# Optimization experiments

Hardware: AMD Instinct MI355X
Metric: run time of the kernel (lower is better)

Reference implementation:

```python
import jax, jax.numpy as jnp
import numpy as np

N, D, K, H, G = 200000, 256, 128, 4, 1024  # nodes, emb_dim, hidden, heads, graphs


def setup_inputs() -> dict:
    key = jax.random.key(0)
    k0, k1, k2, k3 = jax.random.split(key, 4)
    node_features = jax.random.normal(k0, (N, D), jnp.float32)
    segment_ids = jnp.sort(jax.random.randint(k1, (N,), 0, G)).astype(jnp.int32)
    W1 = jax.random.normal(k2, (H, D, K), jnp.float32) / np.float32(np.sqrt(D))
    b1 = jnp.zeros((H, K), jnp.float32)
    W2 = jax.random.normal(k3, (H, K), jnp.float32) / np.float32(np.sqrt(K))
    b2 = jnp.zeros((H,), jnp.float32)
    return {"node_features": node_features, "segment_ids": segment_ids,
            "num_graphs": G, "W1": W1, "b1": b1, "W2": W2, "b2": b2}


def _segment_softmax(scores, seg, num_segments):
    # scores: [N, H]; numerically-stable softmax within each graph segment, per head
    m = jax.ops.segment_max(scores, seg, num_segments=num_segments)  # [G, H]
    e = jnp.exp(scores - m[seg])
    s = jax.ops.segment_sum(e, seg, num_segments=num_segments)  # [G, H]
    return e / s[seg]


def reference(node_features, segment_ids, num_graphs, W1, b1, W2, b2):
    # Per-head MLP score for all heads at once: [N, H]
    h = jax.nn.relu(jnp.einsum('nd,hdk->nhk', node_features, W1) + b1)
    scores = jnp.einsum('nhk,hk->nh', h, W2) + b2
    # dgl.softmax_nodes per head == segment softmax over graph ids
    attn = _segment_softmax(scores, segment_ids, num_graphs)  # [N, H]
    # combine_type == 'mean': mean_h segment_sum(attn_h * x)
    # == segment_sum(mean_h(attn_h) * x) since the sum is linear in attn.
    avg_attn = attn.mean(axis=1)  # [N]
    weighted = avg_attn[:, None] * node_features  # [N, D]
    return jax.ops.segment_sum(weighted, segment_ids, num_segments=num_graphs)  # [G, D]
```

## Files before the change

### kernel.cpp

```cpp
#include <hip/hip_runtime.h>
#include <hip/hip_bf16.h>

typedef unsigned short u16;
typedef __attribute__((ext_vector_type(8))) __bf16 bf16x8;
typedef __attribute__((ext_vector_type(8))) u16 u16x8;
typedef __attribute__((ext_vector_type(4))) float f32x4;

__device__ __forceinline__ u16 f2bf(float f) {
    unsigned u = __float_as_uint(f);
    u += 0x7fffu + ((u >> 16) & 1u);
    return (u16)(u >> 16);
}

__device__ __forceinline__ void gl_lds16(const void* g, void* l) {
    __builtin_amdgcn_global_load_lds(
        (const __attribute__((address_space(1))) void*)g,
        (__attribute__((address_space(3))) void*)l, 16, 0, 0);
}

__device__ __forceinline__ bf16x8 cvt8(f32x4 lo, f32x4 hi) {
    u16x8 u;
    u[0] = f2bf(lo[0]); u[1] = f2bf(lo[1]); u[2] = f2bf(lo[2]); u[3] = f2bf(lo[3]);
    u[4] = f2bf(hi[0]); u[5] = f2bf(hi[1]); u[6] = f2bf(hi[2]); u[7] = f2bf(hi[3]);
    return __builtin_bit_cast(bf16x8, u);
}

__global__ __launch_bounds__(256) void transpose_w1(const float* __restrict__ W1,
                                                    u16* __restrict__ W1T) {
    int idx = blockIdx.x * 256 + threadIdx.x;
    int h = idx >> 15;
    int rem = idx & 32767;
    int k = rem >> 8;
    int d = rem & 255;
    float v = W1[((size_t)h * 256 + d) * 128 + k];
    W1T[idx] = f2bf(v);
}

__global__ __launch_bounds__(256, 3) void score_kernel(
        const float* __restrict__ x, const u16* __restrict__ W1T,
        const float* __restrict__ b1, const float* __restrict__ W2,
        const float* __restrict__ b2, float* __restrict__ scores, int N) {
    __shared__ char sA[2][8192];
    __shared__ char sB[2][16384];
    __shared__ float red[2][128];

    const int t = threadIdx.x;
    const int wave = t >> 6;
    const int lane = t & 63;
    const int l15 = lane & 15;
    const int quad = lane >> 4;
    const int n0 = blockIdx.x * 128;
    const int h = blockIdx.y;
    const int valid = min(128, N - n0);

    const char* Abase = (const char*)(W1T + (size_t)h * 128 * 256);
    const char* Xbase = (const char*)x;

    f32x4 acc[4][4] = {};
    const int wr = (wave & 1) * 64;
    const int wn = (wave >> 1) * 64;

    auto stage = [&](int it, int buf) {
        const int k0 = it * 32;
#pragma unroll
        for (int j = 0; j < 2; ++j) {
            int s = j * 256 + t;
            int r = s >> 2, c = s & 3;
            const char* g = Abase + (size_t)r * 512 + k0 * 2 + ((c ^ ((r >> 1) & 3)) * 16);
            gl_lds16(g, &sA[buf][j * 4096 + wave * 1024]);
        }
#pragma unroll
        for (int j = 0; j < 4; ++j) {
            int s = j * 256 + t;
            int n = s >> 3, c = s & 7;
            int nn = n0 + n; if (nn >= N) nn = N - 1;
            const char* g = Xbase + (size_t)nn * 1024 + k0 * 4 + ((c ^ (n & 7)) * 16);
            gl_lds16(g, &sB[buf][j * 4096 + wave * 1024]);
        }
    };

    stage(0, 0);
    __syncthreads();

    for (int it = 0; it < 8; ++it) {
        if (it < 7) stage(it + 1, (it + 1) & 1);
        const int buf = it & 1;
        bf16x8 a[4], b[4];
#pragma unroll
        for (int rt = 0; rt < 4; ++rt) {
            int rl = wr + rt * 16 + l15;
            a[rt] = *reinterpret_cast<const bf16x8*>(
                &sA[buf][rl * 64 + ((quad ^ ((rl >> 1) & 3)) * 16)]);
        }
#pragma unroll
        for (int nt = 0; nt < 4; ++nt) {
            int nl = wn + nt * 16 + l15;
            f32x4 lo = *reinterpret_cast<const f32x4*>(
                &sB[buf][nl * 128 + (((2 * quad) ^ (nl & 7)) * 16)]);
            f32x4 hi = *reinterpret_cast<const f32x4*>(
                &sB[buf][nl * 128 + (((2 * quad + 1) ^ (nl & 7)) * 16)]);
            b[nt] = cvt8(lo, hi);
        }
#pragma unroll
        for (int rt = 0; rt < 4; ++rt)
#pragma unroll
            for (int nt = 0; nt < 4; ++nt)
                acc[rt][nt] = __builtin_amdgcn_mfma_f32_16x16x32_bf16(
                    a[rt], b[nt], acc[rt][nt], 0, 0, 0);
        __syncthreads();
    }

    float part[4] = {0.f, 0.f, 0.f, 0.f};
#pragma unroll
    for (int rt = 0; rt < 4; ++rt) {
        int rb = wr + rt * 16 + quad * 4;
        float4 w2v = *reinterpret_cast<const float4*>(W2 + h * 128 + rb);
        float4 b1v = *reinterpret_cast<const float4*>(b1 + h * 128 + rb);
#pragma unroll
        for (int nt = 0; nt < 4; ++nt) {
            f32x4 c = acc[rt][nt];
            part[nt] += fmaxf(c[0] + b1v.x, 0.f) * w2v.x
                      + fmaxf(c[1] + b1v.y, 0.f) * w2v.y
                      + fmaxf(c[2] + b1v.z, 0.f) * w2v.z
                      + fmaxf(c[3] + b1v.w, 0.f) * w2v.w;
        }
    }
#pragma unroll
    for (int nt = 0; nt < 4; ++nt) {
        float p = part[nt];
        p += __shfl_xor(p, 16, 64);
        p += __shfl_xor(p, 32, 64);
        if (lane < 16) red[wave & 1][wn + nt * 16 + l15] = p;
    }
    __syncthreads();
    if (t < valid)
        scores[(size_t)(n0 + t) * 4 + h] = red[0][t] + red[1][t] + b2[h];
}

__device__ __forceinline__ int lower_bound(const int* __restrict__ a, int n, int v) {
    int lo = 0, hi = n;
    while (lo < hi) {
        int mid = (lo + hi) >> 1;
        if (a[mid] < v) lo = mid + 1; else hi = mid;
    }
    return lo;
}

__global__ __launch_bounds__(256) void segstat_kernel(
        const float4* __restrict__ scores4, const int* __restrict__ seg,
        float4* __restrict__ mOut, float4* __restrict__ isOut, int N) {
    __shared__ float4 redm[4];
    __shared__ float4 reds[4];
    const int g = blockIdx.x;
    const int t = threadIdx.x;
    const int start = lower_bound(seg, N, g);
    const int end = lower_bound(seg, N, g + 1);

    float4 mx = make_float4(-3.4e38f, -3.4e38f, -3.4e38f, -3.4e38f);
    for (int i = start + t; i < end; i += 256) {
        float4 s = scores4[i];
        mx.x = fmaxf(mx.x, s.x); mx.y = fmaxf(mx.y, s.y);
        mx.z = fmaxf(mx.z, s.z); mx.w = fmaxf(mx.w, s.w);
    }
#pragma unroll
    for (int off = 1; off < 64; off <<= 1) {
        mx.x = fmaxf(mx.x, __shfl_xor(mx.x, off, 64));
        mx.y = fmaxf(mx.y, __shfl_xor(mx.y, off, 64));
        mx.z = fmaxf(mx.z, __shfl_xor(mx.z, off, 64));
        mx.w = fmaxf(mx.w, __shfl_xor(mx.w, off, 64));
    }
    if ((t & 63) == 0) redm[t >> 6] = mx;
    __syncthreads();
    mx = redm[0];
#pragma unroll
    for (int w = 1; w < 4; ++w) {
        mx.x = fmaxf(mx.x, redm[w].x); mx.y = fmaxf(mx.y, redm[w].y);
        mx.z = fmaxf(mx.z, redm[w].z); mx.w = fmaxf(mx.w, redm[w].w);
    }

    float4 sm = make_float4(0.f, 0.f, 0.f, 0.f);
    for (int i = start + t; i < end; i += 256) {
        float4 s = scores4[i];
        sm.x += expf(s.x - mx.x); sm.y += expf(s.y - mx.y);
        sm.z += expf(s.z - mx.z); sm.w += expf(s.w - mx.w);
    }
#pragma unroll
    for (int off = 1; off < 64; off <<= 1) {
        sm.x += __shfl_xor(sm.x, off, 64);
        sm.y += __shfl_xor(sm.y, off, 64);
        sm.z += __shfl_xor(sm.z, off, 64);
        sm.w += __shfl_xor(sm.w, off, 64);
    }
    if ((t & 63) == 0) reds[t >> 6] = sm;
    __syncthreads();
    if (t == 0) {
        float4 tot = reds[0];
        for (int w = 1; w < 4; ++w) {
            tot.x += reds[w].x; tot.y += reds[w].y;
            tot.z += reds[w].z; tot.w += reds[w].w;
        }
        bool nonempty = end > start;
        float4 m_out = nonempty ? mx : make_float4(0.f, 0.f, 0.f, 0.f);
        float4 is;
        is.x = (nonempty && tot.x > 0.f) ? 1.f / tot.x : 0.f;
        is.y = (nonempty && tot.y > 0.f) ? 1.f / tot.y : 0.f;
        is.z = (nonempty && tot.z > 0.f) ? 1.f / tot.z : 0.f;
        is.w = (nonempty && tot.w > 0.f) ? 1.f / tot.w : 0.f;
        mOut[g] = m_out;
        isOut[g] = is;
    }
}

__global__ __launch_bounds__(256) void wsum_kernel(
        const float* __restrict__ x, const float4* __restrict__ scores4,
        const int* __restrict__ seg, const float4* __restrict__ mArr,
        const float4* __restrict__ isArr, float* __restrict__ out, int N) {
    __shared__ float wl[256];
    __shared__ int gl[256];
    __shared__ unsigned long long bmask[4];
    const int t = threadIdx.x;
    const int n0 = blockIdx.x * 256;
    const int cnt = min(256, N - n0);

    int g = -1;
    float w = 0.f;
    if (t < cnt) {
        int n = n0 + t;
        g = seg[n];
        float4 s = scores4[n];
        float4 m = mArr[g];
        float4 is = isArr[g];
        w = 0.25f * (expf(s.x - m.x) * is.x + expf(s.y - m.y) * is.y +
                     expf(s.z - m.z) * is.z + expf(s.w - m.w) * is.w);
    }
    gl[t] = g;
    wl[t] = w;
    __syncthreads();
    bool bnd = (t > 0) && (t < cnt) && (gl[t] != gl[t - 1]);
    unsigned long long bm = __ballot(bnd);
    if ((t & 63) == 0) bmask[t >> 6] = bm;
    __syncthreads();

    int rs = 0;
    while (rs < cnt) {
        int re = cnt;
        {
            int wd = (rs + 1) >> 6, bb = (rs + 1) & 63;
            for (; wd < 4; ++wd, bb = 0) {
                unsigned long long mm = bmask[wd];
                if (bb) mm &= (~0ULL) << bb;
                if (mm) { re = wd * 64 + (__ffsll(mm) - 1); break; }
            }
            if (re > cnt) re = cnt;
        }
        float acc = 0.f;
        int i = rs;
        for (; i + 8 <= re; i += 8) {
            float xv[8];
#pragma unroll
            for (int j = 0; j < 8; ++j)
                xv[j] = x[(size_t)(n0 + i + j) * 256 + t];
#pragma unroll
            for (int j = 0; j < 8; ++j) acc += wl[i + j] * xv[j];
        }
        for (; i < re; ++i) acc += wl[i] * x[(size_t)(n0 + i) * 256 + t];
        atomicAdd(&out[(size_t)gl[rs] * 256 + t], acc);
        rs = re;
    }
}

extern "C" void kernel_launch(void* const* d_in, const int* in_sizes, int n_in,
                              void* d_out, int out_size, void* d_ws, size_t ws_size,
                              hipStream_t stream) {
    const float* x  = (const float*)d_in[0];
    const int* seg  = (const int*)d_in[1];
    const float* W1 = (const float*)d_in[3];
    const float* b1 = (const float*)d_in[4];
    const float* W2 = (const float*)d_in[5];
    const float* b2 = (const float*)d_in[6];
    float* out = (float*)d_out;

    const int N = in_sizes[0] / 256;
    const int G = 1024;

    char* ws = (char*)d_ws;
    float* scores = (float*)ws;
    u16* W1T      = (u16*)(ws + (size_t)N * 16);
    float* mArr   = (float*)(ws + (size_t)N * 16 + 262144);
    float* isArr  = mArr + (size_t)G * 4;

    hipMemsetAsync(d_out, 0, (size_t)G * 256 * sizeof(float), stream);
    transpose_w1<<<512, 256, 0, stream>>>(W1, W1T);
    dim3 sgrid((N + 127) / 128, 4);
    score_kernel<<<sgrid, 256, 0, stream>>>(x, W1T, b1, W2, b2, scores, N);
    segstat_kernel<<<G, 256, 0, stream>>>((const float4*)scores, seg,
                                          (float4*)mArr, (float4*)isArr, N);
    wsum_kernel<<<(N + 255) / 256, 256, 0, stream>>>(x, (const float4*)scores, seg,
                                                     (const float4*)mArr,
                                                     (const float4*)isArr, out, N);
}
```

Baseline: 423.2 us.

## Restructure score GEMM to load x once for all heads, retile wsum

The score kernel now handles 64 nodes per block across all four heads at once, one wave per head. Each block converts its x tile to bf16 a single time in LDS and streams all of W1T through LDS. The old kernel launched one block per head and so read and converted x four times. The W1 transpose now goes through an LDS tile for coalesced access, and wsum uses 64-node blocks with a single ballot mask, which gives more blocks and more atomics.

```diff
diff --git a/kernel.cpp b/kernel.cpp
--- a/kernel.cpp
+++ b/kernel.cpp
@@ -18,123 +18,135 @@
         (__attribute__((address_space(3))) void*)l, 16, 0, 0);
 }
 
-__device__ __forceinline__ bf16x8 cvt8(f32x4 lo, f32x4 hi) {
-    u16x8 u;
-    u[0] = f2bf(lo[0]); u[1] = f2bf(lo[1]); u[2] = f2bf(lo[2]); u[3] = f2bf(lo[3]);
-    u[4] = f2bf(hi[0]); u[5] = f2bf(hi[1]); u[6] = f2bf(hi[2]); u[7] = f2bf(hi[3]);
-    return __builtin_bit_cast(bf16x8, u);
-}
-
 __global__ __launch_bounds__(256) void transpose_w1(const float* __restrict__ W1,
                                                     u16* __restrict__ W1T) {
-    int idx = blockIdx.x * 256 + threadIdx.x;
-    int h = idx >> 15;
-    int rem = idx & 32767;
-    int k = rem >> 8;
-    int d = rem & 255;
-    float v = W1[((size_t)h * 256 + d) * 128 + k];
-    W1T[idx] = f2bf(v);
-}
-
-__global__ __launch_bounds__(256, 3) void score_kernel(
+    __shared__ u16 tile[64][132];
+    const int t = threadIdx.x;
+    const int h = blockIdx.x >> 2;
+    const int dt = blockIdx.x & 3;
+#pragma unroll
+    for (int j = 0; j < 8; ++j) {
+        int idx = j * 256 + t;
+        int r = idx >> 5;
+        int kq = idx & 31;
+        float4 v = *reinterpret_cast<const float4*>(
+            W1 + ((size_t)h * 256 + dt * 64 + r) * 128 + kq * 4);
+        ushort4 o;
+        o.x = f2bf(v.x); o.y = f2bf(v.y); o.z = f2bf(v.z); o.w = f2bf(v.w);
+        *reinterpret_cast<ushort4*>(&tile[r][kq * 4]) = o;
+    }
+    __syncthreads();
+#pragma unroll
+    for (int j = 0; j < 4; ++j) {
+        int idx = j * 256 + t;
+        int k = idx >> 3;
+        int c8 = idx & 7;
+        u16x8 o;
+#pragma unroll
+        for (int e = 0; e < 8; ++e) o[e] = tile[c8 * 8 + e][k];
+        *reinterpret_cast<u16x8*>(W1T + ((size_t)h * 128 + k) * 256 + dt * 64 + c8 * 8) = o;
+    }
+}
+
+__global__ __launch_bounds__(256, 2) void score_kernel(
         const float* __restrict__ x, const u16* __restrict__ W1T,
         const float* __restrict__ b1, const float* __restrict__ W2,
         const float* __restrict__ b2, float* __restrict__ scores, int N) {
-    __shared__ char sA[2][8192];
-    __shared__ char sB[2][16384];
-    __shared__ float red[2][128];
+    __shared__ u16 xb[16384];
+    __shared__ u16 sA[16384];
 
     const int t = threadIdx.x;
     const int wave = t >> 6;
     const int lane = t & 63;
     const int l15 = lane & 15;
     const int quad = lane >> 4;
-    const int n0 = blockIdx.x * 128;
-    const int h = blockIdx.y;
-    const int valid = min(128, N - n0);
-
-    const char* Abase = (const char*)(W1T + (size_t)h * 128 * 256);
-    const char* Xbase = (const char*)x;
-
-    f32x4 acc[4][4] = {};
-    const int wr = (wave & 1) * 64;
-    const int wn = (wave >> 1) * 64;
-
-    auto stage = [&](int it, int buf) {
-        const int k0 = it * 32;
-#pragma unroll
-        for (int j = 0; j < 2; ++j) {
-            int s = j * 256 + t;
-            int r = s >> 2, c = s & 3;
-            const char* g = Abase + (size_t)r * 512 + k0 * 2 + ((c ^ ((r >> 1) & 3)) * 16);
-            gl_lds16(g, &sA[buf][j * 4096 + wave * 1024]);
-        }
-#pragma unroll
-        for (int j = 0; j < 4; ++j) {
-            int s = j * 256 + t;
-            int n = s >> 3, c = s & 7;
-            int nn = n0 + n; if (nn >= N) nn = N - 1;
-            const char* g = Xbase + (size_t)nn * 1024 + k0 * 4 + ((c ^ (n & 7)) * 16);
-            gl_lds16(g, &sB[buf][j * 4096 + wave * 1024]);
+    const int n0 = blockIdx.x * 64;
+
+    {
+        const int nrow = wave * 16 + (lane >> 2);
+        const int koff = (lane & 3) * 8;
+        int nn = n0 + nrow; if (nn >= N) nn = N - 1;
+        const float* src = x + (size_t)nn * 256 + koff;
+        float4 v[16];
+#pragma unroll
+        for (int i = 0; i < 8; ++i) {
+            v[2 * i]     = *reinterpret_cast<const float4*>(src + i * 32);
+            v[2 * i + 1] = *reinterpret_cast<const float4*>(src + i * 32 + 4);
+        }
+#pragma unroll
+        for (int i = 0; i < 8; ++i) {
+            u16x8 o;
+            o[0] = f2bf(v[2*i].x);   o[1] = f2bf(v[2*i].y);
+            o[2] = f2bf(v[2*i].z);   o[3] = f2bf(v[2*i].w);
+            o[4] = f2bf(v[2*i+1].x); o[5] = f2bf(v[2*i+1].y);
+            o[6] = f2bf(v[2*i+1].z); o[7] = f2bf(v[2*i+1].w);
+            *reinterpret_cast<u16x8*>(&xb[(i * 256 + t) * 8]) = o;
+        }
+    }
+
+    const int arr = (lane >> 2);
+    const int akc = (lane & 3) * 8;
+    auto stageA = [&](int ks) {
+        const int k0 = ks * 32;
+#pragma unroll
+        for (int j = 0; j < 8; ++j) {
+            int fr = wave * 8 + j;
+            const u16* g = W1T + (size_t)(fr * 16 + arr) * 256 + k0 + akc;
+            gl_lds16(g, &sA[(size_t)fr * 512]);
         }
     };
 
-    stage(0, 0);
-    __syncthreads();
-
-    for (int it = 0; it < 8; ++it) {
-        if (it < 7) stage(it + 1, (it + 1) & 1);
-        const int buf = it & 1;
-        bf16x8 a[4], b[4];
-#pragma unroll
-        for (int rt = 0; rt < 4; ++rt) {
-            int rl = wr + rt * 16 + l15;
-            a[rt] = *reinterpret_cast<const bf16x8*>(
-                &sA[buf][rl * 64 + ((quad ^ ((rl >> 1) & 3)) * 16)]);
-        }
-#pragma unroll
-        for (int nt = 0; nt < 4; ++nt) {
-            int nl = wn + nt * 16 + l15;
-            f32x4 lo = *reinterpret_cast<const f32x4*>(
-                &sB[buf][nl * 128 + (((2 * quad) ^ (nl & 7)) * 16)]);
-            f32x4 hi = *reinterpret_cast<const f32x4*>(
-                &sB[buf][nl * 128 + (((2 * quad + 1) ^ (nl & 7)) * 16)]);
-            b[nt] = cvt8(lo, hi);
-        }
-#pragma unroll
-        for (int rt = 0; rt < 4; ++rt)
-#pragma unroll
-            for (int nt = 0; nt < 4; ++nt)
-                acc[rt][nt] = __builtin_amdgcn_mfma_f32_16x16x32_bf16(
-                    a[rt], b[nt], acc[rt][nt], 0, 0, 0);
+    f32x4 acc[8][4] = {};
+    stageA(0);
+    __syncthreads();
+
+    for (int ks = 0; ks < 8; ++ks) {
+        bf16x8 a[8], b[4];
+#pragma unroll
+        for (int fr = 0; fr < 8; ++fr)
+            a[fr] = *reinterpret_cast<const bf16x8*>(
+                &sA[((wave * 8 + fr) * 64 + l15 * 4 + quad) * 8]);
+#pragma unroll
+        for (int nf = 0; nf < 4; ++nf)
+            b[nf] = *reinterpret_cast<const bf16x8*>(
+                &xb[((ks * 4 + nf) * 64 + l15 * 4 + quad) * 8]);
         __syncthreads();
-    }
-
-    float part[4] = {0.f, 0.f, 0.f, 0.f};
-#pragma unroll
-    for (int rt = 0; rt < 4; ++rt) {
-        int rb = wr + rt * 16 + quad * 4;
-        float4 w2v = *reinterpret_cast<const float4*>(W2 + h * 128 + rb);
-        float4 b1v = *reinterpret_cast<const float4*>(b1 + h * 128 + rb);
-#pragma unroll
-        for (int nt = 0; nt < 4; ++nt) {
-            f32x4 c = acc[rt][nt];
-            part[nt] += fmaxf(c[0] + b1v.x, 0.f) * w2v.x
-                      + fmaxf(c[1] + b1v.y, 0.f) * w2v.y
-                      + fmaxf(c[2] + b1v.z, 0.f) * w2v.z
-                      + fmaxf(c[3] + b1v.w, 0.f) * w2v.w;
-        }
-    }
-#pragma unroll
-    for (int nt = 0; nt < 4; ++nt) {
-        float p = part[nt];
+        if (ks < 7) stageA(ks + 1);
+#pragma unroll
+        for (int fr = 0; fr < 8; ++fr)
+#pragma unroll
+            for (int nf = 0; nf < 4; ++nf)
+                acc[fr][nf] = __builtin_amdgcn_mfma_f32_16x16x32_bf16(
+                    a[fr], b[nf], acc[fr][nf], 0, 0, 0);
+        __syncthreads();
+    }
+
+    const int h = wave;
+    float4 b1v[8], w2v[8];
+#pragma unroll
+    for (int fr = 0; fr < 8; ++fr) {
+        int rb = h * 128 + fr * 16 + quad * 4;
+        b1v[fr] = *reinterpret_cast<const float4*>(b1 + rb);
+        w2v[fr] = *reinterpret_cast<const float4*>(W2 + rb);
+    }
+    const float b2v = b2[h];
+#pragma unroll
+    for (int nf = 0; nf < 4; ++nf) {
+        float p = 0.f;
+#pragma unroll
+        for (int fr = 0; fr < 8; ++fr) {
+            f32x4 c = acc[fr][nf];
+            p += fmaxf(c[0] + b1v[fr].x, 0.f) * w2v[fr].x
+               + fmaxf(c[1] + b1v[fr].y, 0.f) * w2v[fr].y
+               + fmaxf(c[2] + b1v[fr].z, 0.f) * w2v[fr].z
+               + fmaxf(c[3] + b1v[fr].w, 0.f) * w2v[fr].w;
+        }
         p += __shfl_xor(p, 16, 64);
         p += __shfl_xor(p, 32, 64);
-        if (lane < 16) red[wave & 1][wn + nt * 16 + l15] = p;
-    }
-    __syncthreads();
-    if (t < valid)
-        scores[(size_t)(n0 + t) * 4 + h] = red[0][t] + red[1][t] + b2[h];
+        int n = n0 + nf * 16 + lane;
+        if (lane < 16 && n < N)
+            scores[(size_t)n * 4 + h] = p + b2v;
+    }
 }
 
 __device__ __forceinline__ int lower_bound(const int* __restrict__ a, int n, int v) {
@@ -215,44 +227,40 @@
         const float* __restrict__ x, const float4* __restrict__ scores4,
         const int* __restrict__ seg, const float4* __restrict__ mArr,
         const float4* __restrict__ isArr, float* __restrict__ out, int N) {
-    __shared__ float wl[256];
-    __shared__ int gl[256];
-    __shared__ unsigned long long bmask[4];
+    __shared__ float wl[64];
+    __shared__ int gl[64];
+    __shared__ unsigned long long bmask_s;
     const int t = threadIdx.x;
-    const int n0 = blockIdx.x * 256;
-    const int cnt = min(256, N - n0);
-
-    int g = -1;
-    float w = 0.f;
-    if (t < cnt) {
-        int n = n0 + t;
-        g = seg[n];
-        float4 s = scores4[n];
-        float4 m = mArr[g];
-        float4 is = isArr[g];
-        w = 0.25f * (expf(s.x - m.x) * is.x + expf(s.y - m.y) * is.y +
-                     expf(s.z - m.z) * is.z + expf(s.w - m.w) * is.w);
-    }
-    gl[t] = g;
-    wl[t] = w;
-    __syncthreads();
-    bool bnd = (t > 0) && (t < cnt) && (gl[t] != gl[t - 1]);
-    unsigned long long bm = __ballot(bnd);
-    if ((t & 63) == 0) bmask[t >> 6] = bm;
-    __syncthreads();
+    const int n0 = blockIdx.x * 64;
+    const int cnt = min(64, N - n0);
+
+    if (t < 64) {
+        int g = -1;
+        float w = 0.f;
+        bool bnd = false;
+        if (t < cnt) {
+            int n = n0 + t;
+            g = seg[n];
+            float4 s = scores4[n];
+            float4 m = mArr[g];
+            float4 is = isArr[g];
+            w = 0.25f * (expf(s.x - m.x) * is.x + expf(s.y - m.y) * is.y +
+                         expf(s.z - m.z) * is.z + expf(s.w - m.w) * is.w);
+            bnd = (t > 0) && (g != seg[n - 1]);
+        }
+        wl[t] = w;
+        gl[t] = g;
+        unsigned long long bm = __ballot(bnd);
+        if (t == 0) bmask_s = bm;
+    }
+    __syncthreads();
+    const unsigned long long bmask = bmask_s;
 
     int rs = 0;
     while (rs < cnt) {
-        int re = cnt;
-        {
-            int wd = (rs + 1) >> 6, bb = (rs + 1) & 63;
-            for (; wd < 4; ++wd, bb = 0) {
-                unsigned long long mm = bmask[wd];
-                if (bb) mm &= (~0ULL) << bb;
-                if (mm) { re = wd * 64 + (__ffsll(mm) - 1); break; }
-            }
-            if (re > cnt) re = cnt;
-        }
+        unsigned long long mm = (rs < 63) ? (bmask & ((~0ULL) << (rs + 1))) : 0ULL;
+        int re = mm ? (__ffsll((long long)mm) - 1) : cnt;
+        if (re > cnt) re = cnt;
         float acc = 0.f;
         int i = rs;
         for (; i + 8 <= re; i += 8) {
@@ -290,12 +298,11 @@
     float* isArr  = mArr + (size_t)G * 4;
 
     hipMemsetAsync(d_out, 0, (size_t)G * 256 * sizeof(float), stream);
-    transpose_w1<<<512, 256, 0, stream>>>(W1, W1T);
-    dim3 sgrid((N + 127) / 128, 4);
-    score_kernel<<<sgrid, 256, 0, stream>>>(x, W1T, b1, W2, b2, scores, N);
+    transpose_w1<<<16, 256, 0, stream>>>(W1, W1T);
+    score_kernel<<<(N + 63) / 64, 256, 0, stream>>>(x, W1T, b1, W2, b2, scores, N);
     segstat_kernel<<<G, 256, 0, stream>>>((const float4*)scores, seg,
                                           (float4*)mArr, (float4*)isArr, N);
-    wsum_kernel<<<(N + 255) / 256, 256, 0, stream>>>(x, (const float4*)scores, seg,
-                                                     (const float4*)mArr,
-                                                     (const float4*)isArr, out, N);
-}
+    wsum_kernel<<<(N + 63) / 64, 256, 0, stream>>>(x, (const float4*)scores, seg,
+                                                   (const float4*)mArr,
+                                                   (const float4*)isArr, out, N);
+}
```

After: 383.7 us. 1.1x faster.
